# Optimization experiments

Measured on AMD Instinct MI355X. Metric: run time of the kernel, lower is better.

## Reference

```python
import jax, jax.numpy as jnp
import numpy as np

B, T, C, H = 128, 256, 384, 6
HS = C // H  # 64
EPS = 1e-5


def _ln(x, g, b):
    mu = jnp.mean(x, axis=-1, keepdims=True)
    var = jnp.mean(jnp.square(x - mu), axis=-1, keepdims=True)
    return (x - mu) * jax.lax.rsqrt(var + EPS) * g + b


def setup_inputs() -> dict:
    key = jax.random.key(0)
    ks = jax.random.split(key, 12)
    s = 0.02
    return {
        "x": jax.random.normal(ks[0], (B, T, C), jnp.float32),
        "wq": jax.random.normal(ks[1], (H, C, HS), jnp.float32) * s,
        "wk": jax.random.normal(ks[2], (H, C, HS), jnp.float32) * s,
        "wv": jax.random.normal(ks[3], (H, C, HS), jnp.float32) * s,
        "w_proj": jax.random.normal(ks[4], (C, C), jnp.float32) * s,
        "b_proj": jax.random.normal(ks[5], (C,), jnp.float32) * s,
        "w1": jax.random.normal(ks[6], (C, 4 * C), jnp.float32) * s,
        "b1": jax.random.normal(ks[7], (4 * C,), jnp.float32) * s,
        "w2": jax.random.normal(ks[8], (4 * C, C), jnp.float32) * s,
        "b2": jax.random.normal(ks[9], (C,), jnp.float32) * s,
        "ln1_g": 1.0 + jax.random.normal(ks[10], (C,), jnp.float32) * s,
        "ln1_b": jnp.zeros((C,), jnp.float32),
        "ln2_g": 1.0 + jax.random.normal(ks[11], (C,), jnp.float32) * s,
        "ln2_b": jnp.zeros((C,), jnp.float32),
    }


def reference(x, wq, wk, wv, w_proj, b_proj, w1, b1, w2, b2, ln1_g, ln1_b, ln2_g, ln2_b):
    # --- attention sublayer (dropout = identity, eval mode) ---
    h = _ln(x, ln1_g, ln1_b)                              # (B,T,C)
    q = jnp.einsum("btc,hcd->bhtd", h, wq)               # (B,H,T,HS)
    k = jnp.einsum("btc,hcd->bhtd", h, wk)
    v = jnp.einsum("btc,hcd->bhtd", h, wv)
    # NOTE: original scales by n_embed**-0.5 (C), not head_size**-0.5
    wei = jnp.einsum("bhtd,bhsd->bhts", q, k) * (C ** -0.5)  # (B,H,T,T)
    tril = jnp.tril(jnp.ones((T, T), bool))
    wei = jnp.where(tril, wei, -jnp.inf)
    # NOTE: original applies softmax over torch dim=1 of (B,T,T) = query axis
    wei = jax.nn.softmax(wei, axis=2)
    attn = jnp.einsum("bhts,bhsd->bhtd", wei, v)          # (B,H,T,HS)
    attn = attn.transpose(0, 2, 1, 3).reshape(B, T, C)    # head-concat order
    x = x + attn @ w_proj + b_proj
    # --- MLP sublayer ---
    h2 = _ln(x, ln2_g, ln2_b)
    x = x + jax.nn.relu(h2 @ w1 + b1) @ w2 + b2
    return x
```

## Files before the change

### kernel.cpp

```cpp
#include <hip/hip_runtime.h>

#define BB 128
#define TT 256
#define CCH 384
#define NHH 6
#define HSZ 64
#define BTT (BB*TT)
#define QKVLD 1152

typedef unsigned short u16;
typedef unsigned int   u32;
typedef __attribute__((ext_vector_type(8))) short  short8;
typedef __attribute__((ext_vector_type(4))) float  floatx4;

__device__ __forceinline__ u16 f2bf(float f) {
  union { float f; u32 i; } v; v.f = f; u32 x = v.i;
  return (u16)((x + 0x7fffu + ((x >> 16) & 1u)) >> 16);
}
__device__ __forceinline__ float bf2f(u16 w) {
  union { u32 i; float f; } v; v.i = ((u32)w) << 16; return v.f;
}

__device__ __forceinline__ void gll16(const u16* g, u16* l) {
  __builtin_amdgcn_global_load_lds((const __attribute__((address_space(1))) void*)g,
                                   (__attribute__((address_space(3))) void*)l, 16, 0, 0);
}

template <int INBF>
__global__ __launch_bounds__(256) void ln_kernel(const void* __restrict__ xv,
                                                 const float* __restrict__ g,
                                                 const float* __restrict__ b,
                                                 u16* __restrict__ out) {
  int row = blockIdx.x * 4 + (threadIdx.x >> 6);
  int lane = threadIdx.x & 63;
  float vals[6];
  float sum = 0.f;
  if (INBF) {
    const u16* xr = (const u16*)xv + (size_t)row * CCH;
#pragma unroll
    for (int i = 0; i < 6; ++i) { vals[i] = bf2f(xr[lane + (i << 6)]); sum += vals[i]; }
  } else {
    const float* xr = (const float*)xv + (size_t)row * CCH;
#pragma unroll
    for (int i = 0; i < 6; ++i) { vals[i] = xr[lane + (i << 6)]; sum += vals[i]; }
  }
#pragma unroll
  for (int off = 32; off; off >>= 1) sum += __shfl_xor(sum, off);
  float mean = sum * (1.f / 384.f);
  float vs = 0.f;
#pragma unroll
  for (int i = 0; i < 6; ++i) { float d = vals[i] - mean; vs += d * d; }
#pragma unroll
  for (int off = 32; off; off >>= 1) vs += __shfl_xor(vs, off);
  float rinv = rsqrtf(vs * (1.f / 384.f) + 1e-5f);
  u16* orow = out + (size_t)row * CCH;
#pragma unroll
  for (int i = 0; i < 6; ++i) {
    int c = lane + (i << 6);
    orow[c] = f2bf((vals[i] - mean) * rinv * g[c] + b[c]);
  }
}

__global__ void repack_all(const float* __restrict__ wq, const float* __restrict__ wk,
                           const float* __restrict__ wv, const float* __restrict__ wproj,
                           const float* __restrict__ w1, const float* __restrict__ w2,
                           u16* __restrict__ wqkv_t, u16* __restrict__ wp_t,
                           u16* __restrict__ w1_t, u16* __restrict__ w2_t) {
  int idx = blockIdx.x * 256 + threadIdx.x;
  const int S1 = 442368;
  const int S2 = S1 + 147456;
  const int S3 = S2 + 589824;
  const int S4 = S3 + 589824;
  if (idx < S1) {
    int i = idx, e = i & 7, l = (i >> 3) & 63, r = i >> 9;
    int kt = r % 12, nb = r / 12;
    int n = nb * 16 + (l & 15), k = kt * 32 + (l >> 4) * 8 + e;
    int sel = n / 384, nn = n % 384;
    size_t src = ((size_t)(nn >> 6) * 384 + k) * 64 + (nn & 63);
    float v = (sel == 0) ? wq[src] : (sel == 1) ? wk[src] : wv[src];
    wqkv_t[i] = f2bf(v);
  } else if (idx < S2) {
    int i = idx - S1, e = i & 7, l = (i >> 3) & 63, r = i >> 9;
    int kt = r % 12, nb = r / 12;
    int n = nb * 16 + (l & 15), k = kt * 32 + (l >> 4) * 8 + e;
    wp_t[i] = f2bf(wproj[(size_t)k * 384 + n]);
  } else if (idx < S3) {
    int i = idx - S2, e = i & 7, l = (i >> 3) & 63, r = i >> 9;
    int kt = r % 12, nb = r / 12;
    int n = nb * 16 + (l & 15), k = kt * 32 + (l >> 4) * 8 + e;
    w1_t[i] = f2bf(w1[(size_t)k * 1536 + n]);
  } else if (idx < S4) {
    int i = idx - S3, e = i & 7, l = (i >> 3) & 63, r = i >> 9;
    int kt = r % 48, nb = r / 48;
    int n = nb * 16 + (l & 15), k = kt * 32 + (l >> 4) * 8 + e;
    w2_t[i] = f2bf(w2[(size_t)k * 384 + n]);
  }
}

template <int BIAS, int RES, int RELU, int OUTBF, int RESBF>
__global__ __launch_bounds__(256, 3) void gemm_kres(const u16* __restrict__ A,
                                                    const u16* __restrict__ Bp,
                                                    const float* __restrict__ bias,
                                                    const void* __restrict__ resv,
                                                    void* __restrict__ outv,
                                                    int M, int N) {
  __shared__ __align__(16) u16 Ah[64 * 384];
  const int tid = threadIdx.x;
  const int lane = tid & 63;
  const int w = tid >> 6;
  const int wr = w >> 1, wc = w & 1;

  const int gx = gridDim.x;
  const int nwg = gx * gridDim.y;
  const int bid = blockIdx.y * gx + blockIdx.x;
  const int lin = (bid & 7) * (nwg >> 3) + (bid >> 3);
  const int m0 = (lin / gx) * 64, n0 = (lin % gx) * 128;

  const int lm = lane & 15, qd = lane >> 4;

#pragma unroll
  for (int rnd = 0; rnd < 12; ++rnd) {
    int wbase = rnd * 2048 + w * 512;
    int off = wbase + lane * 8;
    int row = off / 384;
    int slot = (off - row * 384) >> 3;
    const u16* src = A + (size_t)(m0 + row) * 384 + ((slot ^ (row & 7)) << 3);
    gll16(src, &Ah[wbase]);
  }

  const u16* bsrc[4];
#pragma unroll
  for (int j = 0; j < 4; ++j)
    bsrc[j] = Bp + ((size_t)((n0 >> 4) + 4 * wc + j) * 12) * 512 + lane * 8;

  floatx4 acc[2][4];
  floatx4 zero4 = {0.f, 0.f, 0.f, 0.f};
#pragma unroll
  for (int i = 0; i < 2; ++i)
#pragma unroll
    for (int j = 0; j < 4; ++j) acc[i][j] = zero4;

  short8 bA[4], bB[4];
#pragma unroll
  for (int j = 0; j < 4; ++j) bA[j] = *(const short8*)(bsrc[j]);

  asm volatile("s_waitcnt vmcnt(0)" ::: "memory");
  __syncthreads();

#pragma unroll
  for (int k2 = 0; k2 < 6; ++k2) {
    {
      const int kt = 2 * k2;
#pragma unroll
      for (int j = 0; j < 4; ++j) bB[j] = *(const short8*)(bsrc[j] + (kt + 1) * 512);
      short8 af[2];
#pragma unroll
      for (int i = 0; i < 2; ++i) {
        int row = 32 * wr + 16 * i + lm;
        int s = (kt * 4 + qd) ^ (row & 7);
        af[i] = *(const short8*)&Ah[row * 384 + s * 8];
      }
#pragma unroll
      for (int i = 0; i < 2; ++i)
#pragma unroll
        for (int j = 0; j < 4; ++j)
          acc[i][j] = __builtin_amdgcn_mfma_f32_16x16x32_bf16(af[i], bA[j], acc[i][j], 0, 0, 0);
    }
    {
      const int kt = 2 * k2 + 1;
      if (kt < 11) {
#pragma unroll
        for (int j = 0; j < 4; ++j) bA[j] = *(const short8*)(bsrc[j] + (kt + 1) * 512);
      }
      short8 af[2];
#pragma unroll
      for (int i = 0; i < 2; ++i) {
        int row = 32 * wr + 16 * i + lm;
        int s = (kt * 4 + qd) ^ (row & 7);
        af[i] = *(const short8*)&Ah[row * 384 + s * 8];
      }
#pragma unroll
      for (int i = 0; i < 2; ++i)
#pragma unroll
        for (int j = 0; j < 4; ++j)
          acc[i][j] = __builtin_amdgcn_mfma_f32_16x16x32_bf16(af[i], bB[j], acc[i][j], 0, 0, 0);
    }
  }

#pragma unroll
  for (int i = 0; i < 2; ++i) {
    int row0 = m0 + 32 * wr + 16 * i + qd * 4;
#pragma unroll
    for (int j = 0; j < 4; ++j) {
      int col = n0 + 64 * wc + 16 * j + lm;
      float bb = 0.f;
      if (BIAS) bb = bias[col];
#pragma unroll
      for (int r = 0; r < 4; ++r) {
        size_t idx = (size_t)(row0 + r) * N + col;
        float val = acc[i][j][r] + bb;
        if (RES) val += RESBF ? bf2f(((const u16*)resv)[idx]) : ((const float*)resv)[idx];
        if (RELU) val = fmaxf(val, 0.f);
        if (OUTBF) ((u16*)outv)[idx] = f2bf(val);
        else       ((float*)outv)[idx] = val;
      }
    }
  }
}

template <int BIAS, int RES, int RELU, int OUTBF, int RESBF>
__global__ __launch_bounds__(256, 3) void gemm_mfma(const u16* __restrict__ A,
                                                    const u16* __restrict__ Bp,
                                                    const float* __restrict__ bias,
                                                    const void* __restrict__ resv,
                                                    void* __restrict__ outv,
                                                    int M, int N, int K) {
  __shared__ __align__(16) u16 As[2][128 * 32];
  const int tid = threadIdx.x;
  const int lane = tid & 63;
  const int w = tid >> 6;
  const int wr = w >> 1, wc = w & 1;

  const int gx = gridDim.x;
  const int nwg = gx * gridDim.y;
  const int bid = blockIdx.y * gx + blockIdx.x;
  const int lin = (bid & 7) * (nwg >> 3) + (bid >> 3);
  const int m0 = (lin / gx) * 128, n0 = (lin % gx) * 128;

  const int lm = lane & 15, qd = lane >> 4;
  const int KT = K >> 5;

  floatx4 acc[4][4];
  floatx4 zero4 = {0.f, 0.f, 0.f, 0.f};
#pragma unroll
  for (int i = 0; i < 4; ++i)
#pragma unroll
    for (int j = 0; j < 4; ++j) acc[i][j] = zero4;

  const u16* srcA[2];
#pragma unroll
  for (int c = 0; c < 2; ++c) {
    int row = 32 * w + 16 * c + (lane >> 2);
    int ch = (lane & 3) ^ ((row >> 1) & 3);
    srcA[c] = A + (size_t)(m0 + row) * K + ch * 8;
  }
  const int dA = (32 * w) * 32;

  const u16* bsrc[4];
#pragma unroll
  for (int j = 0; j < 4; ++j)
    bsrc[j] = Bp + ((size_t)((n0 >> 4) + 4 * wc + j) * KT) * 512 + lane * 8;

#pragma unroll
  for (int c = 0; c < 2; ++c) gll16(srcA[c], &As[0][dA + 512 * c]);
  short8 bcur[4], bnxt[4];
#pragma unroll
  for (int j = 0; j < 4; ++j) bcur[j] = *(const short8*)(bsrc[j]);

  for (int k0 = 0; k0 < K; k0 += 64) {
    __syncthreads();
    {
      int kn = k0 + 32;
      int kto = (kn >> 5) << 9;
#pragma unroll
      for (int j = 0; j < 4; ++j) bnxt[j] = *(const short8*)(bsrc[j] + kto);
#pragma unroll
      for (int c = 0; c < 2; ++c) gll16(srcA[c] + kn, &As[1][dA + 512 * c]);
      short8 af[4];
#pragma unroll
      for (int i = 0; i < 4; ++i) {
        int rm = 64 * wr + 16 * i + lm;
        af[i] = *(const short8*)&As[0][rm * 32 + (qd ^ ((rm >> 1) & 3)) * 8];
      }
#pragma unroll
      for (int i = 0; i < 4; ++i)
#pragma unroll
        for (int j = 0; j < 4; ++j)
          acc[i][j] = __builtin_amdgcn_mfma_f32_16x16x32_bf16(af[i], bcur[j], acc[i][j], 0, 0, 0);
    }
    __syncthreads();
    {
      int kn = k0 + 64;
      if (kn < K) {
        int kto = (kn >> 5) << 9;
#pragma unroll
        for (int j = 0; j < 4; ++j) bcur[j] = *(const short8*)(bsrc[j] + kto);
#pragma unroll
        for (int c = 0; c < 2; ++c) gll16(srcA[c] + kn, &As[0][dA + 512 * c]);
      }
      short8 af[4];
#pragma unroll
      for (int i = 0; i < 4; ++i) {
        int rm = 64 * wr + 16 * i + lm;
        af[i] = *(const short8*)&As[1][rm * 32 + (qd ^ ((rm >> 1) & 3)) * 8];
      }
#pragma unroll
      for (int i = 0; i < 4; ++i)
#pragma unroll
        for (int j = 0; j < 4; ++j)
          acc[i][j] = __builtin_amdgcn_mfma_f32_16x16x32_bf16(af[i], bnxt[j], acc[i][j], 0, 0, 0);
    }
  }

#pragma unroll
  for (int i = 0; i < 4; ++i) {
    int row0 = m0 + 64 * wr + 16 * i + qd * 4;
#pragma unroll
    for (int j = 0; j < 4; ++j) {
      int col = n0 + 64 * wc + 16 * j + lm;
      float bb = 0.f;
      if (BIAS) bb = bias[col];
#pragma unroll
      for (int r = 0; r < 4; ++r) {
        size_t idx = (size_t)(row0 + r) * N + col;
        float val = acc[i][j][r] + bb;
        if (RES) val += RESBF ? bf2f(((const u16*)resv)[idx]) : ((const float*)resv)[idx];
        if (RELU) val = fmaxf(val, 0.f);
        if (OUTBF) ((u16*)outv)[idx] = f2bf(val);
        else       ((float*)outv)[idx] = val;
      }
    }
  }
}

#define ASCALE 0.051031036307982884f

__global__ __launch_bounds__(1024) void attn_mfma(const u16* __restrict__ qkv,
                                                  u16* __restrict__ out) {
  __shared__ __align__(16) char lds_raw[36864 + 20480 + 2048];
  u16*   Ks       = (u16*)lds_raw;
  u16*   VT       = (u16*)lds_raw;
  float* partials = (float*)(lds_raw + 36864);
  u16*   stage    = (u16*)(lds_raw + 36864);
  float* gmax     = (float*)(lds_raw + 57344);
  float* linv     = (float*)(lds_raw + 58368);

  const int tid = threadIdx.x;
  const int lane = tid & 63;
  const int w = tid >> 6;
  const int lm = lane & 15, qd = lane >> 4;
  const int b = blockIdx.x / NHH, h = blockIdx.x % NHH;
  const size_t rowbase = (size_t)b * TT;
  const u16* qp = qkv + rowbase * QKVLD + h * HSZ;
  const u16* kp = qp + 384;
  const u16* vp = qp + 768;

  {
    int s = tid >> 2, c4 = tid & 3;
    const u16* src = kp + (size_t)s * QKVLD;
    *(uint4*)&Ks[s * 72 + c4 * 8]       = *(const uint4*)(src + c4 * 8);
    *(uint4*)&Ks[s * 72 + (c4 + 4) * 8] = *(const uint4*)(src + (c4 + 4) * 8);
  }
  short8 qf0, qf1;
  {
    const u16* qrow = qp + (size_t)(16 * w + lm) * QKVLD + qd * 8;
    qf0 = *(const short8*)(qrow);
    qf1 = *(const short8*)(qrow + 32);
  }
  __syncthreads();

  floatx4 acc[16];
  floatx4 zero4 = {0.f, 0.f, 0.f, 0.f};
#pragma unroll
  for (int tc = 0; tc < 16; ++tc) acc[tc] = zero4;

#pragma unroll
  for (int tc = 0; tc < 16; ++tc) {
    if (tc <= w) {
      int sr = 16 * tc + lm;
      short8 kf0 = *(const short8*)&Ks[sr * 72 + qd * 8];
      short8 kf1 = *(const short8*)&Ks[sr * 72 + 32 + qd * 8];
      acc[tc] = __builtin_amdgcn_mfma_f32_16x16x32_bf16(qf0, kf0, acc[tc], 0, 0, 0);
      acc[tc] = __builtin_amdgcn_mfma_f32_16x16x32_bf16(qf1, kf1, acc[tc], 0, 0, 0);
    }
  }

  const int rb = 16 * w + qd * 4;
  float pmax[16];
#pragma unroll
  for (int tc = 0; tc < 16; ++tc) {
    float m = -1e30f;
    if (tc <= w) {
      int sc = 16 * tc + lm;
#pragma unroll
      for (int r = 0; r < 4; ++r) {
        float vv = acc[tc][r] * ASCALE;
        vv = (rb + r >= sc) ? vv : -1e30f;
        acc[tc][r] = vv;
        m = fmaxf(m, vv);
      }
    }
    m = fmaxf(m, __shfl_xor(m, 16));
    m = fmaxf(m, __shfl_xor(m, 32));
    pmax[tc] = m;
  }
  if (lane < 16) {
#pragma unroll
    for (int tc = 0; tc < 16; ++tc) partials[w * 256 + tc * 16 + lane] = pmax[tc];
  }
  __syncthreads();
  if (tid < 256) {
    float m = partials[tid];
#pragma unroll
    for (int i = 1; i < 16; ++i) m = fmaxf(m, partials[i * 256 + tid]);
    gmax[tid] = m;
  }
  __syncthreads();

  float psum[16];
#pragma unroll
  for (int tc = 0; tc < 16; ++tc) {
    float s = 0.f;
    if (tc <= w) {
      float gm = gmax[tc * 16 + lm];
#pragma unroll
      for (int r = 0; r < 4; ++r) {
        float e = (acc[tc][r] > -1e29f) ? __expf(acc[tc][r] - gm) : 0.f;
        acc[tc][r] = e;
        s += e;
      }
    }
    s += __shfl_xor(s, 16);
    s += __shfl_xor(s, 32);
    psum[tc] = s;
  }
  if (lane < 16) {
#pragma unroll
    for (int tc = 0; tc < 16; ++tc) partials[w * 256 + tc * 16 + lane] = psum[tc];
  }
  __syncthreads();
  if (tid < 256) {
    float s = partials[tid];
#pragma unroll
    for (int i = 1; i < 16; ++i) s += partials[i * 256 + tid];
    linv[tid] = 1.f / s;
  }
  __syncthreads();

  {
    int s = tid >> 2, dg = (tid & 3) * 16;
    const u16* vrow = vp + (size_t)s * QKVLD + dg;
    u16 tmp[16];
    *(uint4*)&tmp[0] = *(const uint4*)(vrow);
    *(uint4*)&tmp[8] = *(const uint4*)(vrow + 8);
#pragma unroll
    for (int j = 0; j < 16; ++j) VT[(dg + j) * 264 + s] = tmp[j];
  }
  __syncthreads();

  u16* mst = stage + w * 640;
  floatx4 oacc[4];
#pragma unroll
  for (int nt = 0; nt < 4; ++nt) oacc[nt] = zero4;

#pragma unroll
  for (int c = 0; c < 8; ++c) {
    if (2 * c <= w) {
#pragma unroll
      for (int tt = 0; tt < 2; ++tt) {
        int tc = 2 * c + tt;
        float li = (tc <= w) ? linv[tc * 16 + lm] : 0.f;
#pragma unroll
        for (int r = 0; r < 4; ++r) {
          float pv = (tc <= w) ? acc[tc][r] * li : 0.f;
          mst[(qd * 4 + r) * 40 + tt * 16 + lm] = f2bf(pv);
        }
      }
      asm volatile("s_waitcnt lgkmcnt(0)" ::: "memory");
      short8 pf = *(const short8*)&mst[lm * 40 + qd * 8];
#pragma unroll
      for (int nt = 0; nt < 4; ++nt) {
        short8 vf = *(const short8*)&VT[(nt * 16 + lm) * 264 + c * 32 + qd * 8];
        oacc[nt] = __builtin_amdgcn_mfma_f32_16x16x32_bf16(pf, vf, oacc[nt], 0, 0, 0);
      }
      asm volatile("" ::: "memory");
    }
  }

  u16* ob = out + rowbase * CCH + h * HSZ;
#pragma unroll
  for (int nt = 0; nt < 4; ++nt) {
#pragma unroll
    for (int r = 0; r < 4; ++r) {
      int t = 16 * w + qd * 4 + r;
      ob[(size_t)t * CCH + nt * 16 + lm] = f2bf(oacc[nt][r]);
    }
  }
}

extern "C" void kernel_launch(void* const* d_in, const int* in_sizes, int n_in,
                              void* d_out, int out_size, void* d_ws, size_t ws_size,
                              hipStream_t stream) {
  const float* x     = (const float*)d_in[0];
  const float* wq    = (const float*)d_in[1];
  const float* wk    = (const float*)d_in[2];
  const float* wv    = (const float*)d_in[3];
  const float* wproj = (const float*)d_in[4];
  const float* bproj = (const float*)d_in[5];
  const float* w1    = (const float*)d_in[6];
  const float* b1    = (const float*)d_in[7];
  const float* w2    = (const float*)d_in[8];
  const float* b2    = (const float*)d_in[9];
  const float* ln1g  = (const float*)d_in[10];
  const float* ln1b  = (const float*)d_in[11];
  const float* ln2g  = (const float*)d_in[12];
  const float* ln2b  = (const float*)d_in[13];
  float* out = (float*)d_out;
  (void)in_sizes; (void)n_in; (void)out_size; (void)ws_size;

  char* ws = (char*)d_ws;
  size_t off = 0;
  auto alloc = [&](size_t bytes) -> void* {
    void* p = ws + off;
    off += (bytes + 255) & ~(size_t)255;
    return p;
  };

  u16* wqkv_t = (u16*)alloc((size_t)QKVLD * CCH * 2);
  u16* wp_t   = (u16*)alloc((size_t)CCH * CCH * 2);
  u16* w1_t   = (u16*)alloc((size_t)4 * CCH * CCH * 2);
  u16* w2_t   = (u16*)alloc((size_t)CCH * 4 * CCH * 2);
  u16*   h_b  = (u16*)alloc((size_t)BTT * CCH * 2);
  u16*   x2   = (u16*)alloc((size_t)BTT * CCH * 2);
  u16*   qkv_b = (u16*)alloc((size_t)BTT * 4 * CCH * 2);
  u16*   u_b   = qkv_b;

  repack_all<<<6912, 256, 0, stream>>>(wq, wk, wv, wproj, w1, w2,
                                       wqkv_t, wp_t, w1_t, w2_t);

  ln_kernel<0><<<BTT / 4, 256, 0, stream>>>(x, ln1g, ln1b, h_b);

  gemm_kres<0, 0, 0, 1, 0><<<dim3(9, 512), 256, 0, stream>>>(h_b, wqkv_t, nullptr, nullptr,
                                                             qkv_b, BTT, QKVLD);
  attn_mfma<<<BB * NHH, 1024, 0, stream>>>(qkv_b, h_b);

  gemm_kres<1, 1, 0, 1, 0><<<dim3(3, 512), 256, 0, stream>>>(h_b, wp_t, bproj, x, x2,
                                                             BTT, CCH);
  ln_kernel<1><<<BTT / 4, 256, 0, stream>>>(x2, ln2g, ln2b, h_b);

  gemm_kres<1, 0, 1, 1, 0><<<dim3(12, 512), 256, 0, stream>>>(h_b, w1_t, b1, nullptr, u_b,
                                                              BTT, 4 * CCH);
  gemm_mfma<1, 1, 0, 0, 1><<<dim3(3, 256), 256, 0, stream>>>(u_b, w2_t, b2, x2, out,
                                                             BTT, CCH, 4 * CCH);
}
```

Before: 353.6 us.

## Widen K-resident GEMM tiles to 64x192 with 3 waves and kt-major LDS layout

Replaces the 4-wave 64x128 K-resident GEMM with a 3-wave 64x192 variant. Each wave now covers all 64 rows and 64 columns with a 4x4 MFMA accumulator block. The A tile is stored in LDS in a kt-major layout with a new XOR swizzle. The intent is to load the A tile once for more output columns, cutting repeated A traffic and the number of blocks. In exchange, each wave holds more accumulator registers and occupancy drops (launch bounds go from 256,3 to 192,2).

```diff
diff --git a/kernel.cpp b/kernel.cpp
--- a/kernel.cpp
+++ b/kernel.cpp
@@ -98,45 +98,44 @@
 }
 
 template <int BIAS, int RES, int RELU, int OUTBF, int RESBF>
-__global__ __launch_bounds__(256, 3) void gemm_kres(const u16* __restrict__ A,
-                                                    const u16* __restrict__ Bp,
-                                                    const float* __restrict__ bias,
-                                                    const void* __restrict__ resv,
-                                                    void* __restrict__ outv,
-                                                    int M, int N) {
-  __shared__ __align__(16) u16 Ah[64 * 384];
+__global__ __launch_bounds__(192, 2) void gemm_kres3(const u16* __restrict__ A,
+                                                     const u16* __restrict__ Bp,
+                                                     const float* __restrict__ bias,
+                                                     const void* __restrict__ resv,
+                                                     void* __restrict__ outv,
+                                                     int M, int N) {
+  __shared__ __align__(16) u16 Ah[12 * 2048];
   const int tid = threadIdx.x;
   const int lane = tid & 63;
   const int w = tid >> 6;
-  const int wr = w >> 1, wc = w & 1;
 
   const int gx = gridDim.x;
   const int nwg = gx * gridDim.y;
   const int bid = blockIdx.y * gx + blockIdx.x;
   const int lin = (bid & 7) * (nwg >> 3) + (bid >> 3);
-  const int m0 = (lin / gx) * 64, n0 = (lin % gx) * 128;
+  const int m0 = (lin / gx) * 64, n0 = (lin % gx) * 192;
 
   const int lm = lane & 15, qd = lane >> 4;
 
 #pragma unroll
-  for (int rnd = 0; rnd < 12; ++rnd) {
-    int wbase = rnd * 2048 + w * 512;
-    int off = wbase + lane * 8;
-    int row = off / 384;
-    int slot = (off - row * 384) >> 3;
-    const u16* src = A + (size_t)(m0 + row) * 384 + ((slot ^ (row & 7)) << 3);
-    gll16(src, &Ah[wbase]);
+  for (int g = 0; g < 16; ++g) {
+    int call = w * 16 + g;
+    int kt = call >> 2, c = call & 3;
+    int row = 16 * c + (lane >> 2);
+    int ch = (lane & 3) ^ ((row >> 1) & 3);
+    const u16* src = A + (size_t)(m0 + row) * 384 + kt * 32 + ch * 8;
+    gll16(src, &Ah[kt * 2048 + c * 512]);
   }
 
   const u16* bsrc[4];
 #pragma unroll
   for (int j = 0; j < 4; ++j)
-    bsrc[j] = Bp + ((size_t)((n0 >> 4) + 4 * wc + j) * 12) * 512 + lane * 8;
-
-  floatx4 acc[2][4];
+    bsrc[j] = Bp + ((size_t)((n0 >> 4) + 4 * w + j) * 12) * 512 + lane * 8;
+
+  floatx4 acc[4][4];
   floatx4 zero4 = {0.f, 0.f, 0.f, 0.f};
 #pragma unroll
-  for (int i = 0; i < 2; ++i)
+  for (int i = 0; i < 4; ++i)
 #pragma unroll
     for (int j = 0; j < 4; ++j) acc[i][j] = zero4;
 
@@ -153,15 +152,14 @@
       const int kt = 2 * k2;
 #pragma unroll
       for (int j = 0; j < 4; ++j) bB[j] = *(const short8*)(bsrc[j] + (kt + 1) * 512);
-      short8 af[2];
-#pragma unroll
-      for (int i = 0; i < 2; ++i) {
-        int row = 32 * wr + 16 * i + lm;
-        int s = (kt * 4 + qd) ^ (row & 7);
-        af[i] = *(const short8*)&Ah[row * 384 + s * 8];
-      }
-#pragma unroll
-      for (int i = 0; i < 2; ++i)
+      short8 af[4];
+#pragma unroll
+      for (int i = 0; i < 4; ++i) {
+        int rm = 16 * i + lm;
+        af[i] = *(const short8*)&Ah[kt * 2048 + rm * 32 + (qd ^ ((rm >> 1) & 3)) * 8];
+      }
+#pragma unroll
+      for (int i = 0; i < 4; ++i)
 #pragma unroll
         for (int j = 0; j < 4; ++j)
           acc[i][j] = __builtin_amdgcn_mfma_f32_16x16x32_bf16(af[i], bA[j], acc[i][j], 0, 0, 0);
@@ -172,15 +170,14 @@
 #pragma unroll
         for (int j = 0; j < 4; ++j) bA[j] = *(const short8*)(bsrc[j] + (kt + 1) * 512);
       }
-      short8 af[2];
-#pragma unroll
-      for (int i = 0; i < 2; ++i) {
-        int row = 32 * wr + 16 * i + lm;
-        int s = (kt * 4 + qd) ^ (row & 7);
-        af[i] = *(const short8*)&Ah[row * 384 + s * 8];
-      }
-#pragma unroll
-      for (int i = 0; i < 2; ++i)
+      short8 af[4];
+#pragma unroll
+      for (int i = 0; i < 4; ++i) {
+        int rm = 16 * i + lm;
+        af[i] = *(const short8*)&Ah[kt * 2048 + rm * 32 + (qd ^ ((rm >> 1) & 3)) * 8];
+      }
+#pragma unroll
+      for (int i = 0; i < 4; ++i)
 #pragma unroll
         for (int j = 0; j < 4; ++j)
           acc[i][j] = __builtin_amdgcn_mfma_f32_16x16x32_bf16(af[i], bB[j], acc[i][j], 0, 0, 0);
@@ -188,11 +185,11 @@
   }
 
 #pragma unroll
-  for (int i = 0; i < 2; ++i) {
-    int row0 = m0 + 32 * wr + 16 * i + qd * 4;
+  for (int i = 0; i < 4; ++i) {
+    int row0 = m0 + 16 * i + qd * 4;
 #pragma unroll
     for (int j = 0; j < 4; ++j) {
-      int col = n0 + 64 * wc + 16 * j + lm;
+      int col = n0 + 64 * w + 16 * j + lm;
       float bb = 0.f;
       if (BIAS) bb = bias[col];
 #pragma unroll
@@ -530,15 +527,15 @@
 
   ln_kernel<0><<<BTT / 4, 256, 0, stream>>>(x, ln1g, ln1b, h_b);
 
-  gemm_kres<0, 0, 0, 1, 0><<<dim3(9, 512), 256, 0, stream>>>(h_b, wqkv_t, nullptr, nullptr,
-                                                             qkv_b, BTT, QKVLD);
+  gemm_kres3<0, 0, 0, 1, 0><<<dim3(6, 512), 192, 0, stream>>>(h_b, wqkv_t, nullptr, nullptr,
+                                                              qkv_b, BTT, QKVLD);
   attn_mfma<<<BB * NHH, 1024, 0, stream>>>(qkv_b, h_b);
 
-  gemm_kres<1, 1, 0, 1, 0><<<dim3(3, 512), 256, 0, stream>>>(h_b, wp_t, bproj, x, x2,
-                                                             BTT, CCH);
+  gemm_kres3<1, 1, 0, 1, 0><<<dim3(2, 512), 192, 0, stream>>>(h_b, wp_t, bproj, x, x2,
+                                                              BTT, CCH);
   ln_kernel<1><<<BTT / 4, 256, 0, stream>>>(x2, ln2g, ln2b, h_b);
 
-  gemm_kres<1, 0, 1, 1, 0><<<dim3(12, 512), 256, 0, stream>>>(h_b, w1_t, b1, nullptr, u_b,
+  gemm_kres3<1, 0, 1, 1, 0><<<dim3(8, 512), 192, 0, stream>>>(h_b, w1_t, b1, nullptr, u_b,
                                                               BTT, 4 * CCH);
   gemm_mfma<1, 1, 0, 0, 1><<<dim3(3, 256), 256, 0, stream>>>(u_b, w2_t, b2, x2, out,
                                                              BTT, CCH, 4 * CCH);
```

Measured after the change: 338.4 us. -4.3%, faster.
